# Performance work log

Hardware: AMD Instinct MI355X
Metric: run time of the kernel (lower is better)

Reference implementation:

```python
import jax, jax.numpy as jnp
import numpy as np

N_NODES = 100000
N_EDGES = 1000000
D_FEAT = 128
N_ACTIONS = 64


def setup_inputs() -> dict:
    key = jax.random.key(0)
    ks = jax.random.split(key, 8)
    return {
        "x": jax.random.normal(ks[0], (N_NODES, D_FEAT), dtype=jnp.float32),
        "edge_index": jax.random.randint(ks[1], (2, N_EDGES), 0, N_NODES, dtype=jnp.int64),
        "W_gcn": jax.random.normal(ks[2], (D_FEAT, D_FEAT), dtype=jnp.float32) / np.sqrt(D_FEAT),
        "b_gcn": jax.random.normal(ks[3], (D_FEAT,), dtype=jnp.float32) * 0.02,
        "W_high": jax.random.normal(ks[4], (D_FEAT, N_ACTIONS), dtype=jnp.float32) / np.sqrt(D_FEAT),
        "b_high": jax.random.normal(ks[5], (N_ACTIONS,), dtype=jnp.float32) * 0.02,
        "W_low": jax.random.normal(ks[6], (D_FEAT, N_ACTIONS), dtype=jnp.float32) / np.sqrt(D_FEAT),
        "b_low": jax.random.normal(ks[7], (N_ACTIONS,), dtype=jnp.float32) * 0.02,
    }


def gcn_conv(x, edge_index, W, b):
    """PyG GCNConv: add self-loops, symmetric normalization, aggregate, linear."""
    n = x.shape[0]
    loops = jnp.arange(n, dtype=edge_index.dtype)
    src = jnp.concatenate([edge_index[0], loops])  # message sources
    dst = jnp.concatenate([edge_index[1], loops])  # message targets
    # degree of each target node (edge weight 1, incl. self-loop)
    deg = jax.ops.segment_sum(jnp.ones(src.shape[0], dtype=x.dtype), dst, num_segments=n)
    dinv = jax.lax.rsqrt(deg)  # deg >= 1 thanks to self-loops
    norm = dinv[src] * dinv[dst]  # [E+N]
    h = x @ W  # [N, D] dense transform first (cheaper than transforming messages)
    agg = jax.ops.segment_sum(h[src] * norm[:, None], dst, num_segments=n)
    return agg + b


def reference(x, edge_index, W_gcn, b_gcn, W_high, b_high, W_low, b_low):
    h = gcn_conv(x, edge_index, W_gcn, b_gcn)  # [N, D]
    high = h @ W_high + b_high  # [N, A]
    low = h @ W_low + b_low     # [N, A]
    return (high, low)
```

## Files before the change

### kernel.cpp

```cpp
#include <hip/hip_runtime.h>


#define BLOCK 256
#define SB 512
#define NB_MAX 784
#define SLOT 2048

typedef _Float16 half8 __attribute__((ext_vector_type(8)));
typedef _Float16 half4 __attribute__((ext_vector_type(4)));
typedef _Float16 half2v __attribute__((ext_vector_type(2)));
typedef float f32x4 __attribute__((ext_vector_type(4)));


__global__ __launch_bounds__(BLOCK) void k_scatter(
    const int* __restrict__ src, const int* __restrict__ dst, int E,
    const float* __restrict__ Wg, const float* __restrict__ Wh,
    const float* __restrict__ Wl, const float* __restrict__ bg,
    const float* __restrict__ bh, const float* __restrict__ bl,
    _Float16* __restrict__ WfT, float* __restrict__ bf,
    int* __restrict__ cursor, int* __restrict__ ebuf, int NB) {
    int b = blockIdx.x;
    if (b < 16) {
        int r = b * 8 + (threadIdx.x >> 5);
        int c0 = (threadIdx.x & 31) * 4;
        float a0 = 0.f, a1 = 0.f, a2 = 0.f, a3 = 0.f;
        for (int j = 0; j < 128; j++) {
            float wg = Wg[r * 128 + j];
            float4 wc;
            if (c0 < 64) wc = *(const float4*)(Wh + j * 64 + c0);
            else         wc = *(const float4*)(Wl + j * 64 + (c0 - 64));
            a0 += wg * wc.x; a1 += wg * wc.y; a2 += wg * wc.z; a3 += wg * wc.w;
        }
        WfT[(size_t)(c0 + 0) * 128 + r] = (_Float16)a0;
        WfT[(size_t)(c0 + 1) * 128 + r] = (_Float16)a1;
        WfT[(size_t)(c0 + 2) * 128 + r] = (_Float16)a2;
        WfT[(size_t)(c0 + 3) * 128 + r] = (_Float16)a3;
    } else if (b == 16) {
        int c = threadIdx.x;
        if (c < 128) {
            float acc = (c < 64) ? bh[c] : bl[c - 64];
            for (int j = 0; j < 128; j++) {
                float wc = (c < 64) ? Wh[j * 64 + c] : Wl[j * 64 + (c - 64)];
                acc += bg[j] * wc;
            }
            bf[c] = acc;
        }
    } else {
        __shared__ int hist[NB_MAX];
        __shared__ int cur[NB_MAX];
        int blk = b - 17;
        int chunk = (E + SB - 1) / SB;
        int e0 = blk * chunk, e1 = min(E, e0 + chunk);
        for (int i = threadIdx.x; i < NB; i += BLOCK) hist[i] = 0;
        __syncthreads();
        for (int e = e0 + threadIdx.x; e < e1; e += BLOCK)
            atomicAdd(&hist[dst[e] >> 7], 1);
        __syncthreads();
        for (int i = threadIdx.x; i < NB; i += BLOCK) {
            int h = hist[i];
            cur[i] = i * SLOT + (h ? atomicAdd(&cursor[i], h) : 0);
        }
        __syncthreads();
        for (int e = e0 + threadIdx.x; e < e1; e += BLOCK) {
            int d = dst[e], s = src[e];
            int pos = atomicAdd(&cur[d >> 7], 1);
            ebuf[pos] = s | ((d & 127) << 20);
        }
    }
}


__global__ __launch_bounds__(BLOCK) void k_node(const int* __restrict__ ebuf,
                                                const int* __restrict__ cursor,
                                                const float* __restrict__ x,
                                                int2* __restrict__ off2,
                                                int* __restrict__ csr,
                                                _Float16* __restrict__ xh,
                                                int n) {
    __shared__ int cnt[128];
    __shared__ int pre[128];
    __shared__ int cur[128];
    int bkt = blockIdx.x;
    int t = threadIdx.x;
    int node0 = bkt << 7;
    int nn = min(128, n - node0);
    int eb0 = bkt * SLOT;
    int eb1 = eb0 + cursor[bkt];

    if (t < 128) cnt[t] = 0;
    __syncthreads();
    for (int e = eb0 + t; e < eb1; e += BLOCK)
        atomicAdd(&cnt[(ebuf[e] >> 20) & 127], 1);
    __syncthreads();
    if (t < 128) pre[t] = cnt[t];
    __syncthreads();
    for (int ofs = 1; ofs < 128; ofs <<= 1) {
        int v = (t < 128 && t >= ofs) ? pre[t - ofs] : 0;
        __syncthreads();
        if (t < 128) pre[t] += v;
        __syncthreads();
    }
    if (t < 128) cur[t] = pre[t] - cnt[t];
    __syncthreads();
    if (t < nn)
        off2[node0 + t] = make_int2(eb0 + cur[t], eb0 + pre[t]);
    for (int e = eb0 + t; e < eb1; e += BLOCK) {
        int p = ebuf[e];
        int pos = atomicAdd(&cur[(p >> 20) & 127], 1);
        csr[eb0 + pos] = p & 0xFFFFF;
    }
    const float4* xr = (const float4*)(x + (size_t)node0 * 128);
    half4* xw = (half4*)(xh + (size_t)node0 * 128);
    for (int idx = t; idx < nn * 32; idx += BLOCK) {
        int row = idx >> 5;
        float dvL = rsqrtf((float)(cnt[row] + 1));
        float4 v = xr[idx];
        half4 o;
        o.x = (_Float16)(dvL * v.x); o.y = (_Float16)(dvL * v.y);
        o.z = (_Float16)(dvL * v.z); o.w = (_Float16)(dvL * v.w);
        xw[idx] = o;
    }
}


__global__ __launch_bounds__(BLOCK) void k_gf(const int2* __restrict__ off2,
                                              const int* __restrict__ csr,
                                              const _Float16* __restrict__ xh,
                                              const _Float16* __restrict__ WfT,
                                              const float* __restrict__ bf,
                                              float* __restrict__ out, int n) {
    __shared__ _Float16 lds[64 * 128];
    int wave = threadIdx.x >> 6;
    int lane = threadIdx.x & 63;
    int T0 = blockIdx.x * 64;
    int wrow0 = wave * 16;
    int nbase = T0 + wrow0;

    int pidx = min(nbase + (lane & 15), n - 1);
    int2 oe = off2[pidx];

    int sb_cur;
    {
        int beg0 = __builtin_amdgcn_readlane(oe.x, 0);
        sb_cur = csr[beg0 + lane];
    }

    for (int i = 0; i < 16; i++) {
        int inext = (i + 1) & 15;
        int begn = __builtin_amdgcn_readlane(oe.x, inext);
        int sb_next = csr[begn + lane];

        int beg = __builtin_amdgcn_readlane(oe.x, i);
        int end = __builtin_amdgcn_readlane(oe.y, i);
        int deg = end - beg;
        float dv = rsqrtf((float)(deg + 1));

        int r = wrow0 + i;
        int d = min(T0 + r, n - 1);
        half2v sv = ((const half2v*)(xh + (size_t)d * 128))[lane];
        float ax = (float)sv.x, ay = (float)sv.y;

        int b0 = 0;
        do {
            int sb = (b0 == 0) ? sb_cur : csr[beg + b0 + lane];
            int nb = min(64, deg - b0);
            for (int rb = 0; rb < nb; rb += 8) {
                half2v v[8];
                float m[8];
#pragma unroll
                for (int j = 0; j < 8; j++) {
                    int se = __builtin_amdgcn_readlane(sb, rb + j);
                    se = min(max(se, 0), n - 1);
                    v[j] = ((const half2v*)(xh + (size_t)se * 128))[lane];
                    m[j] = (rb + j < nb) ? 1.f : 0.f;
                }
#pragma unroll
                for (int j = 0; j < 8; j++) {
                    ax += m[j] * (float)v[j].x;
                    ay += m[j] * (float)v[j].y;
                }
            }
            b0 += 64;
        } while (b0 < deg);
        sb_cur = sb_next;

        half2v o;
        o.x = (_Float16)(dv * ax);
        o.y = (_Float16)(dv * ay);
        int c = lane >> 2;
        int off_h = (((c ^ (r & 7)) << 3) + ((lane & 3) << 1));
        *(half2v*)(lds + r * 128 + off_h) = o;
    }

    int l15 = lane & 15, lk = lane >> 4;
    half8 a[4];
    {
        int r = wrow0 + l15;
#pragma unroll
        for (int kk = 0; kk < 4; kk++) {
            int ch = (kk * 4 + lk) ^ (l15 & 7);
            a[kk] = *(const half8*)(lds + (size_t)r * 128 + ch * 8);
        }
    }
    f32x4 acc[8];
#pragma unroll
    for (int cf = 0; cf < 8; cf++) acc[cf] = (f32x4){0.f, 0.f, 0.f, 0.f};
#pragma unroll
    for (int kk = 0; kk < 4; kk++) {
#pragma unroll
        for (int cf = 0; cf < 8; cf++) {
            half8 bfr = *(const half8*)(WfT + (size_t)(cf * 16 + l15) * 128 + kk * 32 + lk * 8);
            acc[cf] = __builtin_amdgcn_mfma_f32_16x16x32_f16(a[kk], bfr, acc[cf], 0, 0, 0);
        }
    }
#pragma unroll
    for (int cf = 0; cf < 8; cf++) {
        int c = cf * 16 + l15;
        float bv = bf[c];
        size_t cbase = (c < 64) ? (size_t)c : (size_t)n * 64 + (size_t)(c - 64);
        int r0 = T0 + wrow0 + lk * 4;
#pragma unroll
        for (int j = 0; j < 4; j++) {
            int rr = r0 + j;
            if (rr < n) out[cbase + (size_t)rr * 64] = acc[cf][j] + bv;
        }
    }
}

extern "C" void kernel_launch(void* const* d_in, const int* in_sizes, int n_in,
                              void* d_out, int out_size, void* d_ws, size_t ws_size,
                              hipStream_t stream) {
    const float* x  = (const float*)d_in[0];
    const int*   ei = (const int*)d_in[1];
    const float* Wg = (const float*)d_in[2];
    const float* bg = (const float*)d_in[3];
    const float* Wh = (const float*)d_in[4];
    const float* bh = (const float*)d_in[5];
    const float* Wl = (const float*)d_in[6];
    const float* bl = (const float*)d_in[7];
    float* out = (float*)d_out;

    int n = in_sizes[0] / 128;
    int E = in_sizes[1] / 2;
    const int* src = ei;
    const int* dst = ei + E;
    int NB = (n + 127) >> 7;

#define WS_TAKE(ptr, type, count)                                        \
    ptr = (type*)wsp;                                                    \
    wsp = (char*)(((size_t)(wsp + (size_t)(count) * sizeof(type)) + 255) \
                  & ~(size_t)255)

    char* wsp = (char*)d_ws;
    int*      cursor; WS_TAKE(cursor, int,      NB_MAX);
    int*      ebuf;   WS_TAKE(ebuf,   int,      (size_t)NB_MAX * SLOT);
    int2*     off2;   WS_TAKE(off2,   int2,     n);
    int*      csr;    WS_TAKE(csr,    int,      (size_t)NB_MAX * SLOT);
    _Float16* WfT;    WS_TAKE(WfT,    _Float16, 128 * 128);
    float*    bf;     WS_TAKE(bf,     float,    128);
    _Float16* xh;     WS_TAKE(xh,     _Float16, (size_t)n * 128);

    hipMemsetAsync(cursor, 0, (size_t)NB * 4, stream);
    k_scatter<<<17 + SB, BLOCK, 0, stream>>>(
        src, dst, E, Wg, Wh, Wl, bg, bh, bl, WfT, bf, cursor, ebuf, NB);
    k_node<<<NB, BLOCK, 0, stream>>>(ebuf, cursor, x, off2, csr, xh, n);
    k_gf<<<(n + 63) / 64, BLOCK, 0, stream>>>(off2, csr, xh, WfT, bf, out, n);
}
```

Baseline: 248.4 us.

## Split fused gather+GEMM into one-wave-per-node gather and separate MFMA GEMM kernel

Replaces the fused gather-then-MFMA kernel with two kernels. The first gathers neighbour rows with one wave per destination node, using shuffles instead of readlane and exact-count tails instead of masked loads. The second runs a standalone MFMA GEMM over 128 rows per block from an fp16 intermediate buffer. This targets the load imbalance and serial 16-node loop in each wave of the fused kernel. In exchange it adds an extra launch and a 25.6 MB fp16 round trip through global memory.

```diff
diff --git a/kernel.cpp b/kernel.cpp
--- a/kernel.cpp
+++ b/kernel.cpp
@@ -123,106 +123,128 @@
 }
 
 
-__global__ __launch_bounds__(BLOCK) void k_gf(const int2* __restrict__ off2,
-                                              const int* __restrict__ csr,
-                                              const _Float16* __restrict__ xh,
-                                              const _Float16* __restrict__ WfT,
-                                              const float* __restrict__ bf,
-                                              float* __restrict__ out, int n) {
-    __shared__ _Float16 lds[64 * 128];
+__global__ __launch_bounds__(BLOCK) void k_gather(const int2* __restrict__ off2,
+                                                  const int* __restrict__ csr,
+                                                  const _Float16* __restrict__ xh,
+                                                  _Float16* __restrict__ aggh, int n) {
+    int wave = (blockIdx.x * blockDim.x + threadIdx.x) >> 6;
+    int lane = threadIdx.x & 63;
+    if (wave >= n) return;
+    int d = wave;
+    int2 oe = off2[d];
+    int beg = oe.x, end = oe.y;
+    float dv = rsqrtf((float)(end - beg + 1));
+
+    half2v sv = ((const half2v*)(xh + (size_t)d * 128))[lane];
+    float ax = (float)sv.x, ay = (float)sv.y;
+
+    for (int base = beg; base < end; base += 64) {
+        int cnt = min(64, end - base);
+        int s = 0;
+        if (lane < cnt) s = csr[base + lane];
+        int j = 0;
+        for (; j + 8 <= cnt; j += 8) {
+            int s0 = __shfl(s, j);
+            int s1 = __shfl(s, j + 1);
+            int s2 = __shfl(s, j + 2);
+            int s3 = __shfl(s, j + 3);
+            int s4 = __shfl(s, j + 4);
+            int s5 = __shfl(s, j + 5);
+            int s6 = __shfl(s, j + 6);
+            int s7 = __shfl(s, j + 7);
+            half2v v0 = ((const half2v*)(xh + (size_t)s0 * 128))[lane];
+            half2v v1 = ((const half2v*)(xh + (size_t)s1 * 128))[lane];
+            half2v v2 = ((const half2v*)(xh + (size_t)s2 * 128))[lane];
+            half2v v3 = ((const half2v*)(xh + (size_t)s3 * 128))[lane];
+            half2v v4 = ((const half2v*)(xh + (size_t)s4 * 128))[lane];
+            half2v v5 = ((const half2v*)(xh + (size_t)s5 * 128))[lane];
+            half2v v6 = ((const half2v*)(xh + (size_t)s6 * 128))[lane];
+            half2v v7 = ((const half2v*)(xh + (size_t)s7 * 128))[lane];
+            ax += (float)v0.x + (float)v1.x + (float)v2.x + (float)v3.x
+                + (float)v4.x + (float)v5.x + (float)v6.x + (float)v7.x;
+            ay += (float)v0.y + (float)v1.y + (float)v2.y + (float)v3.y
+                + (float)v4.y + (float)v5.y + (float)v6.y + (float)v7.y;
+        }
+        for (; j + 4 <= cnt; j += 4) {
+            int s0 = __shfl(s, j);
+            int s1 = __shfl(s, j + 1);
+            int s2 = __shfl(s, j + 2);
+            int s3 = __shfl(s, j + 3);
+            half2v v0 = ((const half2v*)(xh + (size_t)s0 * 128))[lane];
+            half2v v1 = ((const half2v*)(xh + (size_t)s1 * 128))[lane];
+            half2v v2 = ((const half2v*)(xh + (size_t)s2 * 128))[lane];
+            half2v v3 = ((const half2v*)(xh + (size_t)s3 * 128))[lane];
+            ax += (float)v0.x + (float)v1.x + (float)v2.x + (float)v3.x;
+            ay += (float)v0.y + (float)v1.y + (float)v2.y + (float)v3.y;
+        }
+        for (; j < cnt; j++) {
+            int s0 = __shfl(s, j);
+            half2v v0 = ((const half2v*)(xh + (size_t)s0 * 128))[lane];
+            ax += (float)v0.x;
+            ay += (float)v0.y;
+        }
+    }
+    half2v o;
+    o.x = (_Float16)(dv * ax);
+    o.y = (_Float16)(dv * ay);
+    ((half2v*)(aggh + (size_t)d * 128))[lane] = o;
+}
+
+
+__global__ __launch_bounds__(BLOCK) void k_final(const _Float16* __restrict__ aggh,
+                                                 const _Float16* __restrict__ WfT,
+                                                 const float* __restrict__ bf,
+                                                 float* __restrict__ out, int n) {
     int wave = threadIdx.x >> 6;
     int lane = threadIdx.x & 63;
-    int T0 = blockIdx.x * 64;
-    int wrow0 = wave * 16;
-    int nbase = T0 + wrow0;
-
-    int pidx = min(nbase + (lane & 15), n - 1);
-    int2 oe = off2[pidx];
-
-    int sb_cur;
-    {
-        int beg0 = __builtin_amdgcn_readlane(oe.x, 0);
-        sb_cur = csr[beg0 + lane];
-    }
-
-    for (int i = 0; i < 16; i++) {
-        int inext = (i + 1) & 15;
-        int begn = __builtin_amdgcn_readlane(oe.x, inext);
-        int sb_next = csr[begn + lane];
-
-        int beg = __builtin_amdgcn_readlane(oe.x, i);
-        int end = __builtin_amdgcn_readlane(oe.y, i);
-        int deg = end - beg;
-        float dv = rsqrtf((float)(deg + 1));
-
-        int r = wrow0 + i;
-        int d = min(T0 + r, n - 1);
-        half2v sv = ((const half2v*)(xh + (size_t)d * 128))[lane];
-        float ax = (float)sv.x, ay = (float)sv.y;
-
-        int b0 = 0;
-        do {
-            int sb = (b0 == 0) ? sb_cur : csr[beg + b0 + lane];
-            int nb = min(64, deg - b0);
-            for (int rb = 0; rb < nb; rb += 8) {
-                half2v v[8];
-                float m[8];
-#pragma unroll
-                for (int j = 0; j < 8; j++) {
-                    int se = __builtin_amdgcn_readlane(sb, rb + j);
-                    se = min(max(se, 0), n - 1);
-                    v[j] = ((const half2v*)(xh + (size_t)se * 128))[lane];
-                    m[j] = (rb + j < nb) ? 1.f : 0.f;
-                }
-#pragma unroll
-                for (int j = 0; j < 8; j++) {
-                    ax += m[j] * (float)v[j].x;
-                    ay += m[j] * (float)v[j].y;
-                }
-            }
-            b0 += 64;
-        } while (b0 < deg);
-        sb_cur = sb_next;
-
-        half2v o;
-        o.x = (_Float16)(dv * ax);
-        o.y = (_Float16)(dv * ay);
-        int c = lane >> 2;
-        int off_h = (((c ^ (r & 7)) << 3) + ((lane & 3) << 1));
-        *(half2v*)(lds + r * 128 + off_h) = o;
-    }
-
-    int l15 = lane & 15, lk = lane >> 4;
-    half8 a[4];
-    {
-        int r = wrow0 + l15;
-#pragma unroll
-        for (int kk = 0; kk < 4; kk++) {
-            int ch = (kk * 4 + lk) ^ (l15 & 7);
-            a[kk] = *(const half8*)(lds + (size_t)r * 128 + ch * 8);
-        }
-    }
-    f32x4 acc[8];
-#pragma unroll
-    for (int cf = 0; cf < 8; cf++) acc[cf] = (f32x4){0.f, 0.f, 0.f, 0.f};
+    int l15 = lane & 15;
+    int lk = lane >> 4;
+    int row_base = blockIdx.x * 128 + wave * 32;
+
+    half8 a[2][4];
+#pragma unroll
+    for (int rf = 0; rf < 2; rf++) {
+        int r = row_base + rf * 16 + l15;
+        if (r >= n) r = n - 1;
+        const _Float16* ap = aggh + (size_t)r * 128 + lk * 8;
+#pragma unroll
+        for (int kk = 0; kk < 4; kk++)
+            a[rf][kk] = *(const half8*)(ap + kk * 32);
+    }
+
+    f32x4 acc[2][8];
+#pragma unroll
+    for (int rf = 0; rf < 2; rf++)
+#pragma unroll
+        for (int cf = 0; cf < 8; cf++)
+            acc[rf][cf] = (f32x4){0.f, 0.f, 0.f, 0.f};
+
 #pragma unroll
     for (int kk = 0; kk < 4; kk++) {
 #pragma unroll
         for (int cf = 0; cf < 8; cf++) {
-            half8 bfr = *(const half8*)(WfT + (size_t)(cf * 16 + l15) * 128 + kk * 32 + lk * 8);
-            acc[cf] = __builtin_amdgcn_mfma_f32_16x16x32_f16(a[kk], bfr, acc[cf], 0, 0, 0);
-        }
-    }
+            const _Float16* bp = WfT + (size_t)(cf * 16 + l15) * 128 + kk * 32 + lk * 8;
+            half8 bfr = *(const half8*)bp;
+#pragma unroll
+            for (int rf = 0; rf < 2; rf++)
+                acc[rf][cf] = __builtin_amdgcn_mfma_f32_16x16x32_f16(
+                    a[rf][kk], bfr, acc[rf][cf], 0, 0, 0);
+        }
+    }
+
 #pragma unroll
     for (int cf = 0; cf < 8; cf++) {
         int c = cf * 16 + l15;
         float bv = bf[c];
         size_t cbase = (c < 64) ? (size_t)c : (size_t)n * 64 + (size_t)(c - 64);
-        int r0 = T0 + wrow0 + lk * 4;
-#pragma unroll
-        for (int j = 0; j < 4; j++) {
-            int rr = r0 + j;
-            if (rr < n) out[cbase + (size_t)rr * 64] = acc[cf][j] + bv;
+#pragma unroll
+        for (int rf = 0; rf < 2; rf++) {
+            int r0 = row_base + rf * 16 + lk * 4;
+#pragma unroll
+            for (int j = 0; j < 4; j++) {
+                int r = r0 + j;
+                if (r < n) out[cbase + (size_t)r * 64] = acc[rf][cf][j] + bv;
+            }
         }
     }
 }
@@ -259,10 +281,13 @@
     _Float16* WfT;    WS_TAKE(WfT,    _Float16, 128 * 128);
     float*    bf;     WS_TAKE(bf,     float,    128);
     _Float16* xh;     WS_TAKE(xh,     _Float16, (size_t)n * 128);
+    _Float16* aggh;   WS_TAKE(aggh,   _Float16, (size_t)n * 128);
 
     hipMemsetAsync(cursor, 0, (size_t)NB * 4, stream);
     k_scatter<<<17 + SB, BLOCK, 0, stream>>>(
         src, dst, E, Wg, Wh, Wl, bg, bh, bl, WfT, bf, cursor, ebuf, NB);
     k_node<<<NB, BLOCK, 0, stream>>>(ebuf, cursor, x, off2, csr, xh, n);
-    k_gf<<<(n + 63) / 64, BLOCK, 0, stream>>>(off2, csr, xh, WfT, bf, out, n);
-}
+    k_gather<<<((size_t)n * 64 + BLOCK - 1) / BLOCK, BLOCK, 0, stream>>>(
+        off2, csr, xh, aggh, n);
+    k_final<<<(n + 127) / 128, BLOCK, 0, stream>>>(aggh, WfT, bf, out, n);
+}
```

Result: no change. 249.9 us (+0.6%).
